# Optimization experiments

Hardware: AMD Instinct MI355X
Metric: run time of the kernel (lower is better)

## Reference

```python
import jax, jax.numpy as jnp
import numpy as np

H, W, WIN = 16, 6, 3  # tile height/width, SSIM window
C1, C2 = 0.01 ** 2, 0.03 ** 2  # kornia ssim constants (max_val=1.0)


def _gauss_kernel3():
    # kornia get_gaussian_kernel2d((3,3),(1.5,1.5)), normalized
    c = jnp.arange(WIN, dtype=jnp.float32) - (WIN - 1) / 2.0
    g = jnp.exp(-(c ** 2) / (2.0 * 1.5 ** 2))
    g = g / g.sum()
    k2 = jnp.outer(g, g)
    return (k2 / k2.sum()).reshape(-1)  # (9,)


def _patches3(x):
    # x: (N,H,W) -> (N,H,W,9) 3x3 reflect-padded neighborhoods (kornia filter2d border 'reflect')
    xp = jnp.pad(x, ((0, 0), (1, 1), (1, 1)), mode='reflect')
    rows = [xp[:, i:i + H, j:j + W] for i in range(WIN) for j in range(WIN)]
    return jnp.stack(rows, axis=-1)


def setup_inputs() -> dict:
    key = jax.random.key(0)
    k1, k2 = jax.random.split(key)
    img_tensor = jax.random.uniform(k1, (1, 1, 1024, 768), dtype=jnp.float32)
    chars = jax.random.uniform(k2, (95, 1, 16, 6), dtype=jnp.float32)
    return {"img_tensor": img_tensor, "chars": chars}


def reference(img_tensor, chars):
    img_h, img_w = img_tensor.shape[-2], img_tensor.shape[-1]
    n_rows, n_cols = img_h // H, img_w // W
    # nn.Unfold(kernel=(H,W), stride=(H,W)): row-major tiles, each flattened (h,w)
    tiles = img_tensor[0, 0].reshape(n_rows, H, n_cols, W).transpose(0, 2, 1, 3)
    tiles = tiles.reshape(-1, H, W)              # (nt,H,W)
    refs = chars[:, 0]                           # (nr,H,W)

    kflat = _gauss_kernel3()                     # (9,)
    Tp = _patches3(tiles)                        # (nt,H,W,9)
    Rp = _patches3(refs)                         # (nr,H,W,9)

    # per-image windowed stats (computed ONCE per tile / per ref)
    mu_t = Tp @ kflat                            # (nt,H,W)
    mu_r = Rp @ kflat                            # (nr,H,W)
    ex2_t = (Tp ** 2) @ kflat
    ex2_r = (Rp ** 2) @ kflat
    sig_t = ex2_t - mu_t ** 2
    sig_r = ex2_r - mu_r ** 2

    # pairwise cross term E[t*r]: contract kernel over the 3x3 window axis
    exr = jnp.einsum('thwk,rhwk->trhw', Tp * kflat, Rp)  # (nt,nr,H,W)

    mt = mu_t[:, None]                           # (nt,1,H,W)
    mr = mu_r[None, :]                           # (1,nr,H,W)
    sig_tr = exr - mt * mr
    num = (2.0 * mt * mr + C1) * (2.0 * sig_tr + C2)
    den = (mt ** 2 + mr ** 2 + C1) * (sig_t[:, None] + sig_r[None, :] + C2)
    scores = (num / den).mean(axis=(2, 3))       # (nt,nr)

    dens_t = tiles.mean(axis=(1, 2))             # (nt,)
    dens_r = refs.mean(axis=(1, 2))              # (nr,)
    scores = scores - 3.0 * jnp.abs(dens_t[:, None] - dens_r[None, :])

    best_indices = jnp.argmax(scores, axis=1)
    return best_indices.reshape(-1, n_cols)
```

## Files before the change

### kernel.cpp

```cpp
#include <hip/hip_runtime.h>
#include <math.h>


static constexpr float kC1 = 1.0e-4f;
static constexpr float kC2 = 9.0e-4f;

struct KF { float k[9]; };

__device__ __forceinline__ int refl(int x, int n) {
  if (x < 0) return -x;
  if (x >= n) return 2 * n - 2 - x;
  return x;
}

__global__ __launch_bounds__(128) void refprep_kernel(
    const float* __restrict__ chars, float* __restrict__ refdata,
    float* __restrict__ densR, KF kf) {
  const int hw = blockIdx.x;
  const int r = threadIdx.x;
  if (r >= 96) return;
  const int half = r / 48;
  const int rloc = r - half * 48;
  const int rp = rloc / 6 + 8 * (rloc % 6);
  float* row = refdata + ((size_t)(hw * 2 + half) * 48 + rp) * 12;
  const int h = hw / 6, w = hw % 6;
  if (r < 95) {
    const float* cb = chars + r * 96;
    float mu = 0.f, ex2 = 0.f;
    float wrv[9];
#pragma unroll
    for (int i = 0; i < 3; ++i) {
      const int hh = refl(h + i - 1, 16);
#pragma unroll
      for (int j = 0; j < 3; ++j) {
        const int ww = refl(w + j - 1, 6);
        const float p = cb[hh * 6 + ww];
        const float kv = kf.k[i * 3 + j];
        wrv[i * 3 + j] = 2.0f * kv * p;
        mu += kv * p;
        ex2 += kv * p * p;
      }
    }
    const float sig = ex2 - mu * mu;
#pragma unroll
    for (int k = 0; k < 9; ++k) row[k] = wrv[k];
    row[9]  = 2.0f * mu;
    row[10] = mu * mu + kC1;
    row[11] = sig + kC2;
  } else {
#pragma unroll
    for (int k = 0; k < 9; ++k) row[k] = 0.f;
    row[9]  = 0.f;
    row[10] = kC1;
    row[11] = kC2;
  }
  if (hw == 0) {
    if (r < 95) {
      float s = 0.f;
      for (int i = 0; i < 96; ++i) s += chars[r * 96 + i];
      densR[r] = s * (1.0f / 96.0f);
    } else {
      densR[r] = 0.f;
    }
  }
}

__device__ __forceinline__ void stage_px(const float* __restrict__ src,
                                         float* dst, int lane) {
  const uintptr_t gs = (uintptr_t)src;
  const uintptr_t ls = (uintptr_t)dst;
#define G_(off) ((const __attribute__((address_space(1))) void*)(gs + (off)))
#define L_(off) ((__attribute__((address_space(3))) void*)(uint32_t)(ls + (off)))
  __builtin_amdgcn_global_load_lds(G_(0    + lane * 16), L_(0),    16, 0, 0);
  __builtin_amdgcn_global_load_lds(G_(1024 + lane * 16), L_(1024), 16, 0, 0);
  __builtin_amdgcn_global_load_lds(G_(2048 + lane * 4),  L_(2048), 4, 0, 0);
#undef G_
#undef L_
}

__global__ __launch_bounds__(512, 4) void ssim_main_kernel(
    const float* __restrict__ img, const float* __restrict__ refdata,
    const float* __restrict__ densR, float2* __restrict__ scratch, KF kf) {
  __shared__ float smem[19968];
  __shared__ float densT[32];
  float* padT = smem;
  float* statT = smem + 4608;

  const int tid = threadIdx.x;
  const int w = tid >> 6;
  const int lane = tid & 63;
  const int tthr = lane >> 3;
  const int rthr = lane & 7;
  const int tl0 = tthr * 4;
  const int blk = blockIdx.x;
  const int row0 = blk >> 3;
  const int colg = (blk >> 1) & 3;
  const int half = blk & 1;
  const int c0 = colg * 32;
  const int hwBase = w * 12;
  float* rbuf = smem + 10752 + w * 1152;

  stage_px(refdata + (size_t)(hwBase * 2 + half) * 576, rbuf, lane);

  for (int idx = tid; idx < 4608; idx += 512) {
    const int c = idx >> 5, tl = idx & 31;
    const int ph = c >> 3, pw = c & 7;
    const int h = refl(ph - 1, 16), ww = refl(pw - 1, 6);
    padT[idx] = img[(row0 * 16 + h) * 768 + (c0 + tl) * 6 + ww];
  }
  __syncthreads();

  if (tid < 32) {
    float s = 0.f;
    for (int h = 0; h < 16; ++h)
      for (int ww = 0; ww < 6; ++ww)
        s += padT[((h + 1) * 8 + (ww + 1)) * 32 + tid];
    densT[tid] = s * (1.0f / 96.0f);
  }
  for (int idx = tid; idx < 3072; idx += 512) {
    const int hw = idx >> 5, tl = idx & 31;
    const int h = hw / 6, ww = hw % 6;
    float mu = 0.f, ex2 = 0.f;
#pragma unroll
    for (int i = 0; i < 3; ++i)
#pragma unroll
      for (int j = 0; j < 3; ++j) {
        const float p = padT[((h + i) * 8 + (ww + j)) * 32 + tl];
        const float kv = kf.k[i * 3 + j];
        mu += kv * p;
        ex2 += kv * p * p;
      }
    statT[idx] = mu;
    statT[3072 + idx] = ex2 - mu * mu;
  }
  __syncthreads();

  float num[4][6], den[4][6];
#pragma unroll
  for (int i = 0; i < 4; ++i)
#pragma unroll
    for (int j = 0; j < 6; ++j) { num[i][j] = 0.f; den[i][j] = 1.f; }

#pragma unroll 1
  for (int it = 0; it < 12; ++it) {
    const int hw = hwBase + it;
    const float* buf = rbuf + (it & 1) * 576;

    if (it < 11) {
      asm volatile("s_waitcnt lgkmcnt(0)" ::: "memory");
      stage_px(refdata + (size_t)((hw + 1) * 2 + half) * 576,
               rbuf + ((it + 1) & 1) * 576, lane);
      asm volatile("s_waitcnt vmcnt(3)" ::: "memory");
    } else {
      asm volatile("s_waitcnt vmcnt(0)" ::: "memory");
    }

    const int h6 = hw / 6, w6 = hw - h6 * 6;
    const int pb = (h6 * 8 + w6) * 32 + tl0;

    float e[4][6];
#pragma unroll
    for (int i = 0; i < 4; ++i)
#pragma unroll
      for (int j = 0; j < 6; ++j) e[i][j] = kC2;

    {
      float tpA[4][4];
      {
        const int off[4] = {0, 32, 64, 256};
#pragma unroll
        for (int k = 0; k < 4; ++k) {
          const float4 t = *(const float4*)&padT[pb + off[k]];
          tpA[k][0] = t.x; tpA[k][1] = t.y; tpA[k][2] = t.z; tpA[k][3] = t.w;
        }
      }
#pragma unroll
      for (int j = 0; j < 6; ++j) {
        const float4 wa = *(const float4*)&buf[(rthr + 8 * j) * 12];
#pragma unroll
        for (int i = 0; i < 4; ++i) {
          e[i][j] = fmaf(tpA[0][i], wa.x, e[i][j]);
          e[i][j] = fmaf(tpA[1][i], wa.y, e[i][j]);
          e[i][j] = fmaf(tpA[2][i], wa.z, e[i][j]);
          e[i][j] = fmaf(tpA[3][i], wa.w, e[i][j]);
        }
      }
    }

    float mu[4], sg[4];
    {
      const float4 m = *(const float4*)&statT[hw * 32 + tl0];
      const float4 s = *(const float4*)&statT[3072 + hw * 32 + tl0];
      mu[0]=m.x; mu[1]=m.y; mu[2]=m.z; mu[3]=m.w;
      sg[0]=s.x; sg[1]=s.y; sg[2]=s.z; sg[3]=s.w;
    }

    {
      float tpB[5][4];
      {
        const int off[5] = {288, 320, 512, 544, 576};
#pragma unroll
        for (int k = 0; k < 5; ++k) {
          const float4 t = *(const float4*)&padT[pb + off[k]];
          tpB[k][0] = t.x; tpB[k][1] = t.y; tpB[k][2] = t.z; tpB[k][3] = t.w;
        }
      }
#pragma unroll
      for (int j = 0; j < 6; ++j) {
        const float4 wb = *(const float4*)&buf[(rthr + 8 * j) * 12 + 4];
        const float4 wc = *(const float4*)&buf[(rthr + 8 * j) * 12 + 8];
#pragma unroll
        for (int i = 0; i < 4; ++i) {
          float ev = e[i][j];
          ev = fmaf(tpB[0][i], wb.x, ev);
          ev = fmaf(tpB[1][i], wb.y, ev);
          ev = fmaf(tpB[2][i], wb.z, ev);
          ev = fmaf(tpB[3][i], wb.w, ev);
          ev = fmaf(tpB[4][i], wc.x, ev);
          const float am = mu[i] * wc.y;
          const float n1 = am + kC1;
          const float n2 = ev - am;
          const float d1 = fmaf(mu[i], mu[i], wc.z);
          const float d2 = sg[i] + wc.w;
          const float nn = n1 * n2;
          const float dd = d1 * d2;
          num[i][j] = fmaf(nn, den[i][j], num[i][j] * dd);
          den[i][j] *= dd;
        }
      }
    }

    if (it == 3 || it == 7) {
#pragma unroll
      for (int i = 0; i < 4; ++i)
#pragma unroll
        for (int j = 0; j < 6; ++j) {
          const float s = __builtin_amdgcn_rcpf(den[i][j]);
          num[i][j] *= s;
          den[i][j] *= s;
        }
    }
  }

  __syncthreads();
  float* sb = smem;
#pragma unroll
  for (int i = 0; i < 4; ++i)
#pragma unroll
    for (int j = 0; j < 6; ++j)
      sb[w * 1568 + (tl0 + i) * 49 + (rthr * 6 + j)] = num[i][j] / den[i][j];
  __syncthreads();

  {
    const int tile = tid >> 4, rt = tid & 15;
    const float dt = densT[tile];
    float best = -1e30f; int bi = 0;
#pragma unroll
    for (int q = 0; q < 3; ++q) {
      const int rr = rt * 3 + q;
      const int rg = half * 48 + rr;
      if (rg < 95) {
        float s = 0.f;
#pragma unroll
        for (int g = 0; g < 8; ++g) s += sb[g * 1568 + tile * 49 + rr];
        s = s * (1.0f / 96.0f) - 3.0f * fabsf(dt - densR[rg]);
        if (s > best) { best = s; bi = rg; }
      }
    }
#pragma unroll
    for (int m = 8; m >= 1; m >>= 1) {
      const float ob = __shfl_xor(best, m, 64);
      const int oi = __shfl_xor(bi, m, 64);
      if (ob > best || (ob == best && oi < bi)) { best = ob; bi = oi; }
    }
    if (rt == 0)
      scratch[half * 8192 + row0 * 128 + c0 + tile] = make_float2(best, (float)bi);
  }
}

__global__ __launch_bounds__(256) void combine_kernel(
    const float2* __restrict__ scratch, int* __restrict__ out) {
  const int t = blockIdx.x * 256 + threadIdx.x;
  const float2 a = scratch[t];
  const float2 b = scratch[8192 + t];
  out[t] = (b.x > a.x) ? (int)b.y : (int)a.y;
}

extern "C" void kernel_launch(void* const* d_in, const int* in_sizes, int n_in,
                              void* d_out, int out_size, void* d_ws, size_t ws_size,
                              hipStream_t stream) {
  (void)in_sizes; (void)n_in; (void)out_size; (void)ws_size;
  const float* img = (const float*)d_in[0];
  const float* chars = (const float*)d_in[1];
  int* out = (int*)d_out;
  float* refdata = (float*)d_ws;
  float* densR = refdata + 110592;
  float2* scratch = (float2*)(refdata + 110688);

  KF kf;
  {
    float gg[3], s = 0.f;
    for (int i = 0; i < 3; ++i) {
      const float c = (float)i - 1.0f;
      gg[i] = expf(-(c * c) / (2.0f * 1.5f * 1.5f));
      s += gg[i];
    }
    float gn[3];
    for (int i = 0; i < 3; ++i) gn[i] = gg[i] / s;
    float k2[9]; float ks = 0.f;
    for (int i = 0; i < 3; ++i)
      for (int j = 0; j < 3; ++j) { k2[i * 3 + j] = gn[i] * gn[j]; ks += k2[i * 3 + j]; }
    for (int k = 0; k < 9; ++k) kf.k[k] = k2[k] / ks;
  }

  hipLaunchKernelGGL(refprep_kernel, dim3(96), dim3(128), 0, stream,
                     chars, refdata, densR, kf);
  hipLaunchKernelGGL(ssim_main_kernel, dim3(512), dim3(512), 0, stream,
                     img, refdata, densR, scratch, kf);
  hipLaunchKernelGGL(combine_kernel, dim3(32), dim3(256), 0, stream,
                     scratch, out);
}
```

Before: 59.04 us.

## Accumulate SSIM ratios with Newton-refined reciprocal and strength-reduce loop indexing

Drops the deferred-fraction accumulation (num/den products with periodic renormalisation) and instead accumulates each SSIM term directly as nn times a Newton-refined fast reciprocal of dd. This removes the extra multiplies per element and the renormalisation passes, at the cost of an rcp plus two FMAs per element. It also strength-reduces the per-iteration index math (no divide by 6, incremental pointers), drops the lgkmcnt wait before staging, and swaps the launch-bounds occupancy hint for amdgpu_waves_per_eu(4,4). Removing the lgkmcnt wait could risk a race on the LDS buffer being overwritten, and the refined reciprocal may differ slightly in precision from the old exact final divide.

```diff
diff --git a/kernel.cpp b/kernel.cpp
--- a/kernel.cpp
+++ b/kernel.cpp
@@ -78,7 +78,9 @@
 #undef L_
 }
 
-__global__ __launch_bounds__(512, 4) void ssim_main_kernel(
+__global__ __launch_bounds__(512)
+__attribute__((amdgpu_waves_per_eu(4, 4)))
+void ssim_main_kernel(
     const float* __restrict__ img, const float* __restrict__ refdata,
     const float* __restrict__ densR, float2* __restrict__ scratch, KF kf) {
   __shared__ float smem[19968];
@@ -135,28 +137,28 @@
   }
   __syncthreads();
 
-  float num[4][6], den[4][6];
+  float score[4][6];
 #pragma unroll
   for (int i = 0; i < 4; ++i)
 #pragma unroll
-    for (int j = 0; j < 6; ++j) { num[i][j] = 0.f; den[i][j] = 1.f; }
+    for (int j = 0; j < 6; ++j) score[i][j] = 0.f;
+
+  int pb = (2 * w) * 8 * 32 + tl0;
+  int sbase = hwBase * 32 + tl0;
+  const float* refsrc = refdata + (size_t)((hwBase + 1) * 2 + half) * 576;
+  int w6 = 0;
 
 #pragma unroll 1
   for (int it = 0; it < 12; ++it) {
-    const int hw = hwBase + it;
     const float* buf = rbuf + (it & 1) * 576;
 
     if (it < 11) {
-      asm volatile("s_waitcnt lgkmcnt(0)" ::: "memory");
-      stage_px(refdata + (size_t)((hw + 1) * 2 + half) * 576,
-               rbuf + ((it + 1) & 1) * 576, lane);
+      stage_px(refsrc, rbuf + ((it + 1) & 1) * 576, lane);
       asm volatile("s_waitcnt vmcnt(3)" ::: "memory");
     } else {
       asm volatile("s_waitcnt vmcnt(0)" ::: "memory");
     }
-
-    const int h6 = hw / 6, w6 = hw - h6 * 6;
-    const int pb = (h6 * 8 + w6) * 32 + tl0;
+    refsrc += 1152;
 
     float e[4][6];
 #pragma unroll
@@ -187,12 +189,14 @@
       }
     }
 
-    float mu[4], sg[4];
+    float mu[4], sg[4], mt2[4];
     {
-      const float4 m = *(const float4*)&statT[hw * 32 + tl0];
-      const float4 s = *(const float4*)&statT[3072 + hw * 32 + tl0];
+      const float4 m = *(const float4*)&statT[sbase];
+      const float4 s = *(const float4*)&statT[3072 + sbase];
       mu[0]=m.x; mu[1]=m.y; mu[2]=m.z; mu[3]=m.w;
       sg[0]=s.x; sg[1]=s.y; sg[2]=s.z; sg[3]=s.w;
+#pragma unroll
+      for (int i = 0; i < 4; ++i) mt2[i] = mu[i] * mu[i];
     }
 
     {
@@ -220,26 +224,20 @@
           const float am = mu[i] * wc.y;
           const float n1 = am + kC1;
           const float n2 = ev - am;
-          const float d1 = fmaf(mu[i], mu[i], wc.z);
+          const float d1 = mt2[i] + wc.z;
           const float d2 = sg[i] + wc.w;
           const float nn = n1 * n2;
           const float dd = d1 * d2;
-          num[i][j] = fmaf(nn, den[i][j], num[i][j] * dd);
-          den[i][j] *= dd;
+          const float r0v = __builtin_amdgcn_rcpf(dd);
+          const float r1v = r0v * fmaf(-dd, r0v, 2.0f);
+          score[i][j] = fmaf(nn, r1v, score[i][j]);
         }
       }
     }
 
-    if (it == 3 || it == 7) {
-#pragma unroll
-      for (int i = 0; i < 4; ++i)
-#pragma unroll
-        for (int j = 0; j < 6; ++j) {
-          const float s = __builtin_amdgcn_rcpf(den[i][j]);
-          num[i][j] *= s;
-          den[i][j] *= s;
-        }
-    }
+    pb += (w6 == 5) ? 96 : 32;
+    w6 = (w6 == 5) ? 0 : w6 + 1;
+    sbase += 32;
   }
 
   __syncthreads();
@@ -248,7 +246,7 @@
   for (int i = 0; i < 4; ++i)
 #pragma unroll
     for (int j = 0; j < 6; ++j)
-      sb[w * 1568 + (tl0 + i) * 49 + (rthr * 6 + j)] = num[i][j] / den[i][j];
+      sb[w * 1568 + (tl0 + i) * 49 + (rthr * 6 + j)] = score[i][j];
   __syncthreads();
 
   {
```

Result: slower. 63.04 us (+6.8%).
